# Optimization experiments

Hardware: AMD Instinct MI355X
Metric: run time of the kernel (lower is better)

## Reference

```python
import jax, jax.numpy as jnp
import numpy as np


def setup_inputs() -> dict:
    key = jax.random.key(0)
    k1, k2 = jax.random.split(key)
    n_tokens, embed_dim, num_embed = 16384, 512, 2048
    encode = jax.random.normal(k1, (n_tokens, embed_dim), dtype=jnp.float32)
    # Embedding init in torch: uniform(-1/num_embed, 1/num_embed)
    templat = jax.random.uniform(
        k2, (num_embed, embed_dim), dtype=jnp.float32,
        minval=-1.0 / num_embed, maxval=1.0 / num_embed)
    return {"encode": encode, "templat": templat}


def reference(encode, templat):
    # match_encode_with_templat, eval path: sample=False, detach='encode', metric='l2'
    encode_d = jax.lax.stop_gradient(encode)
    # squared L2 distance: ||e||^2 - 2 e@t^T + ||t||^2 ; logits = -dist
    e_sq = jnp.sum(encode_d * encode_d, axis=-1, keepdims=True)       # (N, 1)
    t_sq = jnp.sum(templat * templat, axis=-1)[None, :]               # (1, M)
    dist = e_sq - 2.0 * (encode_d @ templat.T) + t_sq                 # (N, M)
    logits = -dist
    zsoft = jax.nn.softmax(logits, axis=-1)
    zidx = jnp.argmax(zsoft, axis=-1)                                 # (N,)
    quant = templat[zidx]                                             # (N, C) gather
    return quant, zidx
```

## Files before the change

kernel.cpp:

```cpp
#include <hip/hip_runtime.h>
#include <stdint.h>

#define N_TOK  16384
#define EMB    512
#define NEMB   2048
#define NCHUNK 32
#define CWIN   2.5e-4f
#define WCAP   524288
#define EPAD   19

typedef __attribute__((ext_vector_type(8))) short s16x8;
typedef __attribute__((ext_vector_type(4))) float f32x4;

__device__ __forceinline__ unsigned short f2bf(float f) {
  unsigned u = __float_as_uint(f);
  u += 0x7fffu + ((u >> 16) & 1u);
  return (unsigned short)(u >> 16);
}
__device__ __forceinline__ unsigned mapf(float f) {
  unsigned u = __float_as_uint(f);
  return (u >> 31) ? ~u : (u | 0x80000000u);
}
__device__ __forceinline__ float unmapf(unsigned u) {
  return __uint_as_float((u >> 31) ? (u & 0x7fffffffu) : ~u);
}

__device__ __forceinline__ float pairwise512_sq(const float* se, int lane) {
  int l = lane & 31;
  int b = l >> 3, j = l & 7;
  const float* base = se + b * 128 + j;
  float x = base[0];
  float r = __fmul_rn(x, x);
#pragma unroll
  for (int k = 1; k < 16; ++k) {
    float y = base[8 * k];
    r = __fadd_rn(r, __fmul_rn(y, y));
  }
  r = __fadd_rn(r, __shfl_xor(r, 1));
  r = __fadd_rn(r, __shfl_xor(r, 2));
  r = __fadd_rn(r, __shfl_xor(r, 4));
  r = __fadd_rn(r, __shfl_xor(r, 8));
  r = __fadd_rn(r, __shfl_xor(r, 16));
  return r;
}

__global__ __launch_bounds__(256) void prep_kernel(
    const float* __restrict__ tmp, const float* __restrict__ enc,
    unsigned short* __restrict__ thi, float* __restrict__ tsq,
    unsigned short* __restrict__ ehi, float* __restrict__ esq,
    int* __restrict__ wcount) {
  __shared__ float se[4][EMB];
  int wv = threadIdx.x >> 6, lane = threadIdx.x & 63;
  int row = blockIdx.x * 4 + wv;
  if (blockIdx.x == 0 && threadIdx.x == 0) *wcount = 0;
  bool isT = row < NEMB;
  const float* src = isT ? (tmp + (size_t)row * EMB)
                         : (enc + (size_t)(row - NEMB) * EMB);
  const float4* p = (const float4*)src + lane * 2;
  float4 v0 = p[0], v1 = p[1];
  float f[8] = {v0.x, v0.y, v0.z, v0.w, v1.x, v1.y, v1.z, v1.w};
  unsigned h[8];
#pragma unroll
  for (int i = 0; i < 8; ++i) { h[i] = f2bf(f[i]); se[wv][lane * 8 + i] = f[i]; }
  uint4 packed = { h[0] | (h[1] << 16), h[2] | (h[3] << 16),
                   h[4] | (h[5] << 16), h[6] | (h[7] << 16) };
  unsigned short* dsth = isT ? (thi + (size_t)row * EMB)
                             : (ehi + (size_t)(row - NEMB) * EMB);
  ((uint4*)dsth)[lane] = packed;
  __syncthreads();
  float s = pairwise512_sq(se[wv], lane);
  if (lane == 0) { if (isT) tsq[row] = s; else esq[row - NEMB] = s; }
}

__global__ __launch_bounds__(256, 3) void score_kernel(
    const unsigned short* __restrict__ ehi, const unsigned short* __restrict__ thi,
    const float* __restrict__ tsq,
    unsigned long long* __restrict__ keyc, unsigned* __restrict__ s2c) {
  __shared__ __align__(16) char smem[32768];
  uint4* sA = (uint4*)smem;
  uint4* sB = (uint4*)(smem + 16384);
  const int tid = threadIdx.x, w = tid >> 6, lane = tid & 63;
  const int q = lane >> 4, r = lane & 15;
  const int tokb = (int)blockIdx.x >> 4;
  const int mb   = (int)blockIdx.x & 15;

  f32x4 acc[4][4];
#pragma unroll
  for (int ti = 0; ti < 4; ++ti)
#pragma unroll
    for (int j = 0; j < 4; ++j) acc[ti][j] = (f32x4){0.f, 0.f, 0.f, 0.f};

  for (int kb = 0; kb < 8; ++kb) {
    const int colb = kb * 64;
#pragma unroll
    for (int n = 0; n < 4; ++n) {
      int p = w + n * 4, tile = p >> 1, ks = p & 1;
      const unsigned short* ga =
          ehi + (size_t)(tokb * 128 + tile * 16 + r) * EMB + colb + ks * 32 + q * 8;
      __builtin_amdgcn_global_load_lds(
          (const __attribute__((address_space(1))) void*)ga,
          (__attribute__((address_space(3))) void*)&sA[(tile * 2 + ks) * 64], 16, 0, 0);
      const unsigned short* gb =
          thi + (size_t)(mb * 128 + tile * 16 + r) * EMB + colb + ks * 32 + q * 8;
      __builtin_amdgcn_global_load_lds(
          (const __attribute__((address_space(1))) void*)gb,
          (__attribute__((address_space(3))) void*)&sB[(tile * 2 + ks) * 64], 16, 0, 0);
    }
    __syncthreads();
#pragma unroll
    for (int ks = 0; ks < 2; ++ks) {
      s16x8 af[4], bfr[4];
#pragma unroll
      for (int ti = 0; ti < 4; ++ti)
        af[ti] = ((const s16x8*)sA)[((((w >> 1) * 4 + ti) * 2 + ks) << 6) + lane];
#pragma unroll
      for (int j = 0; j < 4; ++j)
        bfr[j] = ((const s16x8*)sB)[((((w & 1) * 4 + j) * 2 + ks) << 6) + lane];
#pragma unroll
      for (int ti = 0; ti < 4; ++ti)
#pragma unroll
        for (int j = 0; j < 4; ++j)
          acc[ti][j] = __builtin_amdgcn_mfma_f32_16x16x32_bf16(af[ti], bfr[j],
                                                               acc[ti][j], 0, 0, 0);
    }
    __syncthreads();
  }

  unsigned long long* K1 = (unsigned long long*)smem;
  unsigned* S2 = (unsigned*)(smem + 128 * EPAD * 8);
  float tq[4]; int mbase[4];
#pragma unroll
  for (int j = 0; j < 4; ++j) {
    mbase[j] = mb * 128 + ((w & 1) * 4 + j) * 16 + r;
    tq[j] = tsq[mbase[j]];
  }
#pragma unroll
  for (int phase = 0; phase < 2; ++phase) {
    if ((w & 1) == phase) {
#pragma unroll
      for (int ti = 0; ti < 4; ++ti) {
#pragma unroll
        for (int i = 0; i < 4; ++i) {
          unsigned long long k1 = ~0ULL; unsigned s2m = 0xffffffffu;
#pragma unroll
          for (int j = 0; j < 4; ++j) {
            float s = tq[j] - 2.0f * acc[ti][j][i];
            unsigned sm = mapf(s);
            unsigned long long k = ((unsigned long long)sm << 32) | (unsigned)mbase[j];
            if (k < k1) { unsigned o = (unsigned)(k1 >> 32); s2m = o < s2m ? o : s2m; k1 = k; }
            else s2m = sm < s2m ? sm : s2m;
          }
          int tl = (w >> 1) * 64 + ti * 16 + q * 4 + i;
          K1[tl * EPAD + r] = k1;
          S2[tl * EPAD + r] = s2m;
        }
      }
    }
    __syncthreads();
    if (tid < 128) {
      int tl = tid;
      unsigned long long K = ~0ULL; unsigned S = 0xffffffffu;
#pragma unroll
      for (int rr = 0; rr < 16; ++rr) {
        unsigned long long k = K1[tl * EPAD + rr];
        unsigned s2 = S2[tl * EPAD + rr];
        if (k < K) { unsigned o = (unsigned)(K >> 32); S = o < S ? o : S; K = k; }
        else { unsigned o = (unsigned)(k >> 32); S = o < S ? o : S; }
        S = s2 < S ? s2 : S;
      }
      int token = tokb * 128 + tl;
      int chunk = mb * 2 + phase;
      keyc[(size_t)chunk * N_TOK + token] = K;
      s2c [(size_t)chunk * N_TOK + token] = S;
    }
    __syncthreads();
  }
}

__global__ __launch_bounds__(64) void merge_kernel(
    const unsigned long long* __restrict__ keyc, const unsigned* __restrict__ s2c,
    int* __restrict__ bestIdx, int* __restrict__ flag, int* __restrict__ work,
    int* __restrict__ wcount, unsigned long long* __restrict__ rkey) {
  int t = blockIdx.x * 64 + threadIdx.x;
  if (t >= N_TOK) return;
  rkey[t] = ~0ULL;
  unsigned long long K = ~0ULL; unsigned S = 0xffffffffu;
  for (int c = 0; c < NCHUNK; ++c) {
    unsigned long long k = keyc[(size_t)c * N_TOK + t];
    unsigned s2 = s2c[(size_t)c * N_TOK + t];
    if (k < K) { unsigned o = (unsigned)(K >> 32); S = o < S ? o : S; K = k; }
    else { unsigned o = (unsigned)(k >> 32); S = o < S ? o : S; }
    S = s2 < S ? s2 : S;
  }
  float best_f   = unmapf((unsigned)(K >> 32));
  float second_f = unmapf(S);
  int idx = (int)(unsigned)(K & 0xffffffffu);
  bestIdx[t] = idx;
  bool ok = (second_f - best_f >= CWIN) && (idx >= 0) && (idx < NEMB) && (best_f == best_f);
  flag[t] = ok ? 0 : 1;
  if (!ok) {
    bool nanCase = !(best_f == best_f);
    float limit = best_f + CWIN;
    for (int c = 0; c < NCHUNK; ++c) {
      float cf = unmapf((unsigned)(keyc[(size_t)c * N_TOK + t] >> 32));
      if (nanCase || !(cf > limit)) {
        int pos = atomicAdd(wcount, 1);
        if (pos < WCAP) work[pos] = t * NCHUNK + c;
      }
    }
  }
}

__global__ __launch_bounds__(256) void refine_kernel(
    const float* __restrict__ enc, const float* __restrict__ tmp,
    const float* __restrict__ esq, const float* __restrict__ tsq,
    const int* __restrict__ work, const int* __restrict__ wcount,
    unsigned long long* __restrict__ rkey) {
  int total = *wcount; if (total > WCAP) total = WCAP;
  __shared__ float se[EMB];
  const int wv = threadIdx.x >> 6, lane = threadIdx.x & 63;
  for (int p = blockIdx.x; p < total; p += gridDim.x) {
    __syncthreads();
    int item = work[p];
    int token = item / NCHUNK, c = item % NCHUNK;
    const float4* erow = (const float4*)(enc + (size_t)token * EMB);
    for (int i = threadIdx.x; i < 128; i += 256) ((float4*)se)[i] = erow[i];
    __syncthreads();
    float e2 = esq[token];
    unsigned long long lkey = ~0ULL;
#pragma unroll
    for (int j = 0; j < 16; ++j) {
      int m = c * 64 + wv + j * 4;
      const float4* trow = (const float4*)(tmp + (size_t)m * EMB);
      float4 a0 = trow[lane], a1 = trow[lane + 64];
      float4 b0 = ((const float4*)se)[lane], b1 = ((const float4*)se)[lane + 64];
      double s = (double)a0.x * b0.x + (double)a0.y * b0.y
               + (double)a0.z * b0.z + (double)a0.w * b0.w
               + (double)a1.x * b1.x + (double)a1.y * b1.y
               + (double)a1.z * b1.z + (double)a1.w * b1.w;
#pragma unroll
      for (int mask = 1; mask < 64; mask <<= 1) s += __shfl_xor(s, mask);
      if (lane == 0) {
        float M  = (float)s;
        float d1 = __fadd_rn(e2, -__fmul_rn(2.0f, M));
        float d2 = __fadd_rn(d1, tsq[m]);
        unsigned long long key =
            ((unsigned long long)__float_as_uint(d2) << 32) | (unsigned)m;
        if (key < lkey) lkey = key;
      }
    }
    if (lane == 0 && lkey != ~0ULL) atomicMin(&rkey[token], lkey);
  }
}

__global__ void gather_kernel(const float* __restrict__ tmp, const int* __restrict__ bestIdx,
                              const int* __restrict__ flag,
                              const unsigned long long* __restrict__ rkey,
                              float* __restrict__ out) {
  int token = blockIdx.x * 4 + (threadIdx.x >> 6);
  int lane = threadIdx.x & 63;
  int idx = flag[token] ? (int)(unsigned)(rkey[token] & 0xffffffffULL) : bestIdx[token];
  idx = idx < 0 ? 0 : (idx > NEMB - 1 ? NEMB - 1 : idx);
  const float4* src = (const float4*)(tmp + (size_t)idx * EMB) + lane * 2;
  float4* dst = (float4*)(out + (size_t)token * EMB) + lane * 2;
  dst[0] = src[0];
  dst[1] = src[1];
  if (lane == 0) out[(size_t)N_TOK * EMB + token] = (float)idx;
}

extern "C" void kernel_launch(void* const* d_in, const int* in_sizes, int n_in,
                              void* d_out, int out_size, void* d_ws, size_t ws_size,
                              hipStream_t stream) {
  const float* enc = (const float*)d_in[0];
  const float* tmp = (const float*)d_in[1];
  float* out = (float*)d_out;
  char* ws = (char*)d_ws;
  unsigned short* thi = (unsigned short*)ws;
  unsigned short* ehi = (unsigned short*)(ws + 2097152);
  float* tsq      = (float*)(ws + 18874368);
  float* esq      = (float*)(ws + 18882560);
  unsigned long long* keyc = (unsigned long long*)(ws + 18948096);
  unsigned* s2c   = (unsigned*)(ws + 23142400);
  int*   bestIdx  = (int*)  (ws + 25239552);
  int*   flag     = (int*)  (ws + 25305088);
  unsigned long long* rkey = (unsigned long long*)(ws + 25370624);
  int*   wcount   = (int*)  (ws + 25501696);
  int*   work     = (int*)  (ws + 25501760);

  prep_kernel  <<<4608,      256, 0, stream>>>(tmp, enc, thi, tsq, ehi, esq, wcount);
  score_kernel <<<2048,      256, 0, stream>>>(ehi, thi, tsq, keyc, s2c);
  merge_kernel <<<N_TOK/64,  64,  0, stream>>>(keyc, s2c, bestIdx, flag, work, wcount, rkey);
  refine_kernel<<<1024,      256, 0, stream>>>(enc, tmp, esq, tsq, work, wcount, rkey);
  gather_kernel<<<N_TOK/4,   256, 0, stream>>>(tmp, bestIdx, flag, rkey, out);
}
```

Baseline: 223.8 us.

## Rewrite score GEMM as 256x256 tile with double-buffered LDS pipeline

Replaces the 128x128-tile score kernel with a 512-thread, 256x256 tile version. It uses double-buffered LDS staging through global_load_lds with an XOR swizzle, and interleaves loads with MFMA halves using barriers, explicit vmcnt waits and setprio. The per-token argmin/second-min reduction moves from an LDS round-trip to wave shuffles. The aim is to hide global load latency and raise arithmetic intensity. In exchange it uses 128 KB of LDS and many accumulator registers, which limits occupancy, and the hand-tuned wait counts must stay correct.

```diff
diff --git a/kernel.cpp b/kernel.cpp
--- a/kernel.cpp
+++ b/kernel.cpp
@@ -7,7 +7,6 @@
 #define NCHUNK 32
 #define CWIN   2.5e-4f
 #define WCAP   524288
-#define EPAD   19
 
 typedef __attribute__((ext_vector_type(8))) short s16x8;
 typedef __attribute__((ext_vector_type(4))) float f32x4;
@@ -72,109 +71,159 @@
   if (lane == 0) { if (isT) tsq[row] = s; else esq[row - NEMB] = s; }
 }
 
-__global__ __launch_bounds__(256, 3) void score_kernel(
+__global__ __launch_bounds__(512, 2) void score_kernel(
     const unsigned short* __restrict__ ehi, const unsigned short* __restrict__ thi,
     const float* __restrict__ tsq,
     unsigned long long* __restrict__ keyc, unsigned* __restrict__ s2c) {
-  __shared__ __align__(16) char smem[32768];
-  uint4* sA = (uint4*)smem;
-  uint4* sB = (uint4*)(smem + 16384);
+  __shared__ __align__(16) char smem[131072];
   const int tid = threadIdx.x, w = tid >> 6, lane = tid & 63;
   const int q = lane >> 4, r = lane & 15;
-  const int tokb = (int)blockIdx.x >> 4;
-  const int mb   = (int)blockIdx.x & 15;
-
-  f32x4 acc[4][4];
-#pragma unroll
-  for (int ti = 0; ti < 4; ++ti)
-#pragma unroll
-    for (int j = 0; j < 4; ++j) acc[ti][j] = (f32x4){0.f, 0.f, 0.f, 0.f};
-
-  for (int kb = 0; kb < 8; ++kb) {
-    const int colb = kb * 64;
-#pragma unroll
-    for (int n = 0; n < 4; ++n) {
-      int p = w + n * 4, tile = p >> 1, ks = p & 1;
-      const unsigned short* ga =
-          ehi + (size_t)(tokb * 128 + tile * 16 + r) * EMB + colb + ks * 32 + q * 8;
-      __builtin_amdgcn_global_load_lds(
-          (const __attribute__((address_space(1))) void*)ga,
-          (__attribute__((address_space(3))) void*)&sA[(tile * 2 + ks) * 64], 16, 0, 0);
-      const unsigned short* gb =
-          thi + (size_t)(mb * 128 + tile * 16 + r) * EMB + colb + ks * 32 + q * 8;
-      __builtin_amdgcn_global_load_lds(
-          (const __attribute__((address_space(1))) void*)gb,
-          (__attribute__((address_space(3))) void*)&sB[(tile * 2 + ks) * 64], 16, 0, 0);
+  const int wr = w >> 2, wc = w & 3;
+  const int tokb = (int)blockIdx.x >> 3;
+  const int nb   = (int)blockIdx.x & 7;
+
+  const int c0 = tid, c1 = 512 + tid;
+  const int L0 = (c0 * 16) ^ ((((c0 * 16) >> 9) & 1) << 5);
+  const int L1 = (c1 * 16) ^ ((((c1 * 16) >> 9) & 1) << 5);
+  const int row0 = L0 >> 6, ce0 = (L0 & 63) >> 1;
+  const int row1 = L1 >> 6, ce1 = (L1 & 63) >> 1;
+  const unsigned short* pa0 = ehi + (size_t)(tokb * 256 + row0) * EMB + ce0;
+  const unsigned short* pa1 = ehi + (size_t)(tokb * 256 + row1) * EMB + ce1;
+  const unsigned short* pb0 = thi + (size_t)(nb  * 256 + row0) * EMB + ce0;
+  const unsigned short* pb1 = thi + (size_t)(nb  * 256 + row1) * EMB + ce1;
+
+#define STAGE_A(ktp, kk) do {                                                     \
+    char* lb_ = smem + ((((ktp) & 1) * 2 + (kk)) << 14) + (w << 10);              \
+    __builtin_amdgcn_global_load_lds(                                             \
+        (const __attribute__((address_space(1))) void*)(pa0 + (ktp) * 64 + (kk) * 32), \
+        (__attribute__((address_space(3))) void*)lb_, 16, 0, 0);                  \
+    __builtin_amdgcn_global_load_lds(                                             \
+        (const __attribute__((address_space(1))) void*)(pa1 + (ktp) * 64 + (kk) * 32), \
+        (__attribute__((address_space(3))) void*)(lb_ + 8192), 16, 0, 0);         \
+  } while (0)
+#define STAGE_B(ktp, kk) do {                                                     \
+    char* lb_ = smem + 65536 + ((((ktp) & 1) * 2 + (kk)) << 14) + (w << 10);      \
+    __builtin_amdgcn_global_load_lds(                                             \
+        (const __attribute__((address_space(1))) void*)(pb0 + (ktp) * 64 + (kk) * 32), \
+        (__attribute__((address_space(3))) void*)lb_, 16, 0, 0);                  \
+    __builtin_amdgcn_global_load_lds(                                             \
+        (const __attribute__((address_space(1))) void*)(pb1 + (ktp) * 64 + (kk) * 32), \
+        (__attribute__((address_space(3))) void*)(lb_ + 8192), 16, 0, 0);         \
+  } while (0)
+
+  int offA[8], offB[4];
+#pragma unroll
+  for (int m = 0; m < 8; ++m) {
+    int P = (wr * 128 + m * 16 + r) * 64 + q * 16;
+    offA[m] = P ^ (((P >> 9) & 1) << 5);
+  }
+#pragma unroll
+  for (int n = 0; n < 4; ++n) {
+    int P = (wc * 64 + n * 16 + r) * 64 + q * 16;
+    offB[n] = P ^ (((P >> 9) & 1) << 5);
+  }
+
+  f32x4 acc[8][4];
+#pragma unroll
+  for (int m = 0; m < 8; ++m)
+#pragma unroll
+    for (int n = 0; n < 4; ++n) acc[m][n] = (f32x4){0.f, 0.f, 0.f, 0.f};
+
+  STAGE_A(0, 0); STAGE_B(0, 0); STAGE_A(0, 1); STAGE_B(0, 1); STAGE_A(1, 0); STAGE_B(1, 0);
+  asm volatile("s_waitcnt vmcnt(8)" ::: "memory");
+  __builtin_amdgcn_s_barrier();
+
+#define LOADA(kkbase, mh)                                        \
+    a0 = *(const s16x8*)(Ab_ + (kkbase) + offA[(mh) * 4 + 0]);   \
+    a1 = *(const s16x8*)(Ab_ + (kkbase) + offA[(mh) * 4 + 1]);   \
+    a2 = *(const s16x8*)(Ab_ + (kkbase) + offA[(mh) * 4 + 2]);   \
+    a3 = *(const s16x8*)(Ab_ + (kkbase) + offA[(mh) * 4 + 3]);
+#define LOADB(kkbase)                                            \
+    bf4[0] = *(const s16x8*)(Bb_ + (kkbase) + offB[0]);          \
+    bf4[1] = *(const s16x8*)(Bb_ + (kkbase) + offB[1]);          \
+    bf4[2] = *(const s16x8*)(Bb_ + (kkbase) + offB[2]);          \
+    bf4[3] = *(const s16x8*)(Bb_ + (kkbase) + offB[3]);
+#define MFMA_HALF(mh)                                                              \
+    __builtin_amdgcn_s_setprio(1);                                                 \
+    _Pragma("unroll")                                                              \
+    for (int n = 0; n < 4; ++n) {                                                  \
+      acc[(mh) * 4 + 0][n] = __builtin_amdgcn_mfma_f32_16x16x32_bf16(a0, bf4[n], acc[(mh) * 4 + 0][n], 0, 0, 0); \
+      acc[(mh) * 4 + 1][n] = __builtin_amdgcn_mfma_f32_16x16x32_bf16(a1, bf4[n], acc[(mh) * 4 + 1][n], 0, 0, 0); \
+      acc[(mh) * 4 + 2][n] = __builtin_amdgcn_mfma_f32_16x16x32_bf16(a2, bf4[n], acc[(mh) * 4 + 2][n], 0, 0, 0); \
+      acc[(mh) * 4 + 3][n] = __builtin_amdgcn_mfma_f32_16x16x32_bf16(a3, bf4[n], acc[(mh) * 4 + 3][n], 0, 0, 0); \
+    }                                                                              \
+    __builtin_amdgcn_s_setprio(0);
+
+#pragma unroll
+  for (int kt = 0; kt < 8; ++kt) {
+    char* Ab_ = smem + ((kt & 1) * 2 << 14);
+    char* Bb_ = smem + 65536 + ((kt & 1) * 2 << 14);
+    s16x8 a0, a1, a2, a3, bf4[4];
+    LOADA(0, 0); LOADB(0);
+    if (kt + 1 < 8) STAGE_A(kt + 1, 1);
+    __builtin_amdgcn_s_barrier();
+    MFMA_HALF(0);
+    __builtin_amdgcn_s_barrier();
+    LOADA(0, 1);
+    if (kt + 1 < 8) STAGE_B(kt + 1, 1);
+    __builtin_amdgcn_s_barrier();
+    MFMA_HALF(1);
+    if (kt < 7) { asm volatile("s_waitcnt vmcnt(8)" ::: "memory"); }
+    else        { asm volatile("s_waitcnt vmcnt(0)" ::: "memory"); }
+    __builtin_amdgcn_s_barrier();
+    LOADA(16384, 0); LOADB(16384);
+    if (kt + 2 < 8) STAGE_A(kt + 2, 0);
+    __builtin_amdgcn_s_barrier();
+    MFMA_HALF(0);
+    __builtin_amdgcn_s_barrier();
+    LOADA(16384, 1);
+    if (kt + 2 < 8) STAGE_B(kt + 2, 0);
+    __builtin_amdgcn_s_barrier();
+    MFMA_HALF(1);
+    if (kt < 6)       { asm volatile("s_waitcnt vmcnt(8)" ::: "memory"); }
+    else if (kt == 6) { asm volatile("s_waitcnt vmcnt(4)" ::: "memory"); }
+    __builtin_amdgcn_s_barrier();
+  }
+
+  const int chunk = nb * 4 + wc;
+  const int nbase = nb * 256 + wc * 64;
+  float tq[4];
+#pragma unroll
+  for (int n = 0; n < 4; ++n) tq[n] = tsq[nbase + n * 16 + r];
+#pragma unroll
+  for (int m = 0; m < 8; ++m) {
+#pragma unroll
+    for (int i = 0; i < 4; ++i) {
+      unsigned long long k1 = ~0ULL; unsigned s2m = 0xffffffffu;
+#pragma unroll
+      for (int n = 0; n < 4; ++n) {
+        float s = tq[n] - 2.0f * acc[m][n][i];
+        unsigned sm = mapf(s);
+        unsigned long long k =
+            ((unsigned long long)sm << 32) | (unsigned)(nbase + n * 16 + r);
+        if (k < k1) { unsigned o = (unsigned)(k1 >> 32); s2m = o < s2m ? o : s2m; k1 = k; }
+        else s2m = sm < s2m ? sm : s2m;
+      }
+#pragma unroll
+      for (int mask = 1; mask < 16; mask <<= 1) {
+        unsigned long long ok = __shfl_xor(k1, mask);
+        unsigned os = __shfl_xor(s2m, mask);
+        if (ok < k1) { unsigned o = (unsigned)(k1 >> 32); s2m = o < s2m ? o : s2m; k1 = ok; }
+        else { unsigned o = (unsigned)(ok >> 32); s2m = o < s2m ? o : s2m; }
+        s2m = os < s2m ? os : s2m;
+      }
+      if (r == 0) {
+        int token = tokb * 256 + wr * 128 + m * 16 + q * 4 + i;
+        keyc[(size_t)chunk * N_TOK + token] = k1;
+        s2c [(size_t)chunk * N_TOK + token] = s2m;
+      }
     }
-    __syncthreads();
-#pragma unroll
-    for (int ks = 0; ks < 2; ++ks) {
-      s16x8 af[4], bfr[4];
-#pragma unroll
-      for (int ti = 0; ti < 4; ++ti)
-        af[ti] = ((const s16x8*)sA)[((((w >> 1) * 4 + ti) * 2 + ks) << 6) + lane];
-#pragma unroll
-      for (int j = 0; j < 4; ++j)
-        bfr[j] = ((const s16x8*)sB)[((((w & 1) * 4 + j) * 2 + ks) << 6) + lane];
-#pragma unroll
-      for (int ti = 0; ti < 4; ++ti)
-#pragma unroll
-        for (int j = 0; j < 4; ++j)
-          acc[ti][j] = __builtin_amdgcn_mfma_f32_16x16x32_bf16(af[ti], bfr[j],
-                                                               acc[ti][j], 0, 0, 0);
-    }
-    __syncthreads();
-  }
-
-  unsigned long long* K1 = (unsigned long long*)smem;
-  unsigned* S2 = (unsigned*)(smem + 128 * EPAD * 8);
-  float tq[4]; int mbase[4];
-#pragma unroll
-  for (int j = 0; j < 4; ++j) {
-    mbase[j] = mb * 128 + ((w & 1) * 4 + j) * 16 + r;
-    tq[j] = tsq[mbase[j]];
-  }
-#pragma unroll
-  for (int phase = 0; phase < 2; ++phase) {
-    if ((w & 1) == phase) {
-#pragma unroll
-      for (int ti = 0; ti < 4; ++ti) {
-#pragma unroll
-        for (int i = 0; i < 4; ++i) {
-          unsigned long long k1 = ~0ULL; unsigned s2m = 0xffffffffu;
-#pragma unroll
-          for (int j = 0; j < 4; ++j) {
-            float s = tq[j] - 2.0f * acc[ti][j][i];
-            unsigned sm = mapf(s);
-            unsigned long long k = ((unsigned long long)sm << 32) | (unsigned)mbase[j];
-            if (k < k1) { unsigned o = (unsigned)(k1 >> 32); s2m = o < s2m ? o : s2m; k1 = k; }
-            else s2m = sm < s2m ? sm : s2m;
-          }
-          int tl = (w >> 1) * 64 + ti * 16 + q * 4 + i;
-          K1[tl * EPAD + r] = k1;
-          S2[tl * EPAD + r] = s2m;
-        }
-      }
-    }
-    __syncthreads();
-    if (tid < 128) {
-      int tl = tid;
-      unsigned long long K = ~0ULL; unsigned S = 0xffffffffu;
-#pragma unroll
-      for (int rr = 0; rr < 16; ++rr) {
-        unsigned long long k = K1[tl * EPAD + rr];
-        unsigned s2 = S2[tl * EPAD + rr];
-        if (k < K) { unsigned o = (unsigned)(K >> 32); S = o < S ? o : S; K = k; }
-        else { unsigned o = (unsigned)(k >> 32); S = o < S ? o : S; }
-        S = s2 < S ? s2 : S;
-      }
-      int token = tokb * 128 + tl;
-      int chunk = mb * 2 + phase;
-      keyc[(size_t)chunk * N_TOK + token] = K;
-      s2c [(size_t)chunk * N_TOK + token] = S;
-    }
-    __syncthreads();
-  }
+  }
+#undef STAGE_A
+#undef STAGE_B
+#undef LOADA
+#undef LOADB
+#undef MFMA_HALF
 }
 
 __global__ __launch_bounds__(64) void merge_kernel(
@@ -288,7 +337,7 @@
   int*   work     = (int*)  (ws + 25501760);
 
   prep_kernel  <<<4608,      256, 0, stream>>>(tmp, enc, thi, tsq, ehi, esq, wcount);
-  score_kernel <<<2048,      256, 0, stream>>>(ehi, thi, tsq, keyc, s2c);
+  score_kernel <<<512,       512, 0, stream>>>(ehi, thi, tsq, keyc, s2c);
   merge_kernel <<<N_TOK/64,  64,  0, stream>>>(keyc, s2c, bestIdx, flag, work, wcount, rkey);
   refine_kernel<<<1024,      256, 0, stream>>>(enc, tmp, esq, tsq, work, wcount, rkey);
   gather_kernel<<<N_TOK/4,   256, 0, stream>>>(tmp, bestIdx, flag, rkey, out);
```

New measurement: 209.3 us. 6.5% less time.
